# Optimization experiments

Measured on AMD Instinct MI355X. Metric: run time of the kernel, lower is better.

The kernel has to match this reference:

```python
import jax, jax.numpy as jnp
import numpy as np

B, S, D, H = 2, 2048, 1024, 16
HD = D // H
SCALE = float(np.sqrt(HD))


def setup_inputs() -> dict:
    key = jax.random.key(0)
    ks = jax.random.split(key, 11)
    std = 1.0 / np.sqrt(D)
    inp = {
        "query": jax.random.normal(ks[0], (B, S, D), dtype=jnp.float32),
        "key": jax.random.normal(ks[1], (B, S, D), dtype=jnp.float32),
        "value": jax.random.normal(ks[2], (B, S, D), dtype=jnp.float32),
        "w_q": jax.random.normal(ks[3], (D, D), dtype=jnp.float32) * std,
        "b_q": jax.random.normal(ks[4], (D,), dtype=jnp.float32) * std,
        "w_k": jax.random.normal(ks[5], (D, D), dtype=jnp.float32) * std,
        "b_k": jax.random.normal(ks[6], (D,), dtype=jnp.float32) * std,
        "w_v": jax.random.normal(ks[7], (D, D), dtype=jnp.float32) * std,
        "b_v": jax.random.normal(ks[8], (D,), dtype=jnp.float32) * std,
        "w_fc": jax.random.normal(ks[9], (D, D), dtype=jnp.float32) * std,
        "b_fc": jax.random.normal(ks[10], (D,), dtype=jnp.float32) * std,
    }
    return inp


def reference(query, key, value, w_q, b_q, w_k, b_k, w_v, b_v, w_fc, b_fc):
    # Linear projections (torch Linear: x @ W^T + b; here w_* stored as [in, out])
    Q = query @ w_q + b_q            # [B, S, D]
    K = key @ w_k + b_k
    V = value @ w_v + b_v
    # split heads -> [B, H, S, HD]
    Q = Q.reshape(B, S, H, HD).transpose(0, 2, 1, 3)
    K = K.reshape(B, S, H, HD).transpose(0, 2, 1, 3)
    V = V.reshape(B, S, H, HD).transpose(0, 2, 1, 3)
    energy = jnp.einsum('bhqd,bhkd->bhqk', Q, K) / SCALE  # [B, H, S, S]
    attn = jax.nn.softmax(energy, axis=-1)
    x = jnp.einsum('bhqk,bhkd->bhqd', attn, V)            # [B, H, S, HD]
    x = x.transpose(0, 2, 1, 3).reshape(B, S, D)
    return x @ w_fc + b_fc
```

## Files before the change

### kernel.cpp

```cpp
#include <hip/hip_runtime.h>
#include <stdint.h>

#define Bz 2
#define Sz 2048
#define Dz 1024
#define Hz 16
#define HDz 64
#define Mz (Bz*Sz)

typedef unsigned short u16;
typedef __attribute__((ext_vector_type(8))) __bf16 bf16x8;
typedef __attribute__((ext_vector_type(8))) unsigned short u16x8;
typedef __attribute__((ext_vector_type(4))) float f32x4;

#define C1 0.1803368801111243f

__device__ __forceinline__ u16 f2bf(float f) {
  union { float f; unsigned u; } v; v.f = f;
  unsigned r = v.u + 0x7fffu + ((v.u >> 16) & 1u);
  return (u16)(r >> 16);
}

__device__ __forceinline__ unsigned packbf(float a, float b) {
  unsigned ua = __builtin_bit_cast(unsigned, a);
  unsigned ub = __builtin_bit_cast(unsigned, b);
  return ((ua + 0x8000u) >> 16) | ((ub + 0x8000u) & 0xFFFF0000u);
}

__device__ __forceinline__ void async16(void* lds, const void* g) {
  __builtin_amdgcn_global_load_lds(
      (const __attribute__((address_space(1))) unsigned int*)g,
      (__attribute__((address_space(3))) unsigned int*)lds, 16, 0, 0);
}

__global__ void __launch_bounds__(256)
prep_kernel(const float* __restrict__ q, const float* __restrict__ k, const float* __restrict__ v,
            const float* __restrict__ w0, const float* __restrict__ w1,
            const float* __restrict__ w2, const float* __restrict__ w3,
            u16* __restrict__ xq, u16* __restrict__ xk, u16* __restrict__ xv,
            u16* __restrict__ Wt) {
  __shared__ __align__(16) float t[32][33];
  const int bid = blockIdx.x, tid = threadIdx.x;
  if (bid < 12288) {
    const int sel = bid >> 12;
    const int i = ((bid & 4095) << 8) + tid;
    const float* in = sel == 0 ? q : sel == 1 ? k : v;
    u16* out = sel == 0 ? xq : sel == 1 ? xk : xv;
    float4 tv = ((const float4*)in)[i];
    ((ushort4*)out)[i] = make_ushort4(f2bf(tv.x), f2bf(tv.y), f2bf(tv.z), f2bf(tv.w));
  } else {
    const int idx = bid - 12288;
    const int z = idx >> 10, r = idx & 1023;
    const int n0 = (r & 31) * 32, k0 = (r >> 5) * 32;
    const float* W = z == 0 ? w0 : z == 1 ? w1 : z == 2 ? w2 : w3;
    u16* o = Wt + (size_t)z * Dz * Dz;
    const int x = tid & 31, y = tid >> 5;
#pragma unroll
    for (int i = 0; i < 4; ++i)
      t[y + i*8][x] = W[(size_t)(k0 + y + i*8) * Dz + n0 + x];
    __syncthreads();
#pragma unroll
    for (int i = 0; i < 4; ++i)
      o[(size_t)(n0 + y + i*8) * Dz + k0 + x] = f2bf(t[x][y + i*8]);
  }
}

__global__ void __launch_bounds__(256)
gemm_qkv(const u16* __restrict__ xq, const u16* __restrict__ xk, const u16* __restrict__ xv,
         const u16* __restrict__ Wt3,
         const float* __restrict__ bq, const float* __restrict__ bk, const float* __restrict__ bv,
         u16* __restrict__ Qp, u16* __restrict__ Kp, u16* __restrict__ Vt)
{
  __shared__ __align__(16) u16 lA[128][32];
  __shared__ __align__(16) u16 lB[128][32];
  const int sel = blockIdx.x >> 3;
  const int n0 = (blockIdx.x & 7) * 128;
  const int m0 = blockIdx.y * 128;
  const u16* A = sel == 0 ? xq : sel == 1 ? xk : xv;
  const u16* Bt = Wt3 + (size_t)sel * Dz * Dz;
  const float* bias = sel == 0 ? bq : sel == 1 ? bk : bv;

  const int tid = threadIdx.x;
  const int w = tid >> 6, lane = tid & 63;
  const int wm = (w >> 1) * 64, wn = (w & 1) * 64;
  const int l16 = lane & 15, qd = lane >> 4;

  f32x4 acc[4][4];
#pragma unroll
  for (int i = 0; i < 4; ++i)
#pragma unroll
    for (int j = 0; j < 4; ++j) acc[i][j] = (f32x4){0.f, 0.f, 0.f, 0.f};

  const int r0 = tid >> 2, c0 = (tid & 3) * 8;
  const int r1 = r0 + 64;

  for (int k0 = 0; k0 < Dz; k0 += 32) {
    __syncthreads();
    async16(&lA[r0][c0], A  + (size_t)(m0 + r0) * Dz + k0 + c0);
    async16(&lB[r0][c0], Bt + (size_t)(n0 + r0) * Dz + k0 + c0);
    async16(&lA[r1][c0], A  + (size_t)(m0 + r1) * Dz + k0 + c0);
    async16(&lB[r1][c0], Bt + (size_t)(n0 + r1) * Dz + k0 + c0);
    __syncthreads();
    bf16x8 af[4], bfv[4];
#pragma unroll
    for (int t = 0; t < 4; ++t) {
      af[t]  = *(const bf16x8*)&lA[wm + t * 16 + l16][qd * 8];
      bfv[t] = *(const bf16x8*)&lB[wn + t * 16 + l16][qd * 8];
    }
#pragma unroll
    for (int mt = 0; mt < 4; ++mt)
#pragma unroll
      for (int nt = 0; nt < 4; ++nt)
        acc[mt][nt] = __builtin_amdgcn_mfma_f32_16x16x32_bf16(af[mt], bfv[nt], acc[mt][nt], 0, 0, 0);
  }

  if (sel == 2) {
    const int bq2 = m0 >> 11;
    const int s0m = (m0 & 2047) + wm;
#pragma unroll
    for (int nt = 0; nt < 4; ++nt) {
      const int n = n0 + wn + nt * 16 + l16;
      const float bvl = bias[n];
      const int h = n >> 6, hd = n & 63;
      u16* vp = Vt + (size_t)((bq2 * 16 + h) * 64 + hd) * Sz;
#pragma unroll
      for (int mt = 0; mt < 4; ++mt) {
        const int s = s0m + mt * 16 + qd * 4;
        ushort4 o = make_ushort4(f2bf(acc[mt][nt][0] + bvl), f2bf(acc[mt][nt][1] + bvl),
                                 f2bf(acc[mt][nt][2] + bvl), f2bf(acc[mt][nt][3] + bvl));
        *(ushort4*)(vp + s) = o;
      }
    }
  } else {
    u16* Cv = sel == 0 ? Qp : Kp;
#pragma unroll
    for (int nt = 0; nt < 4; ++nt) {
      const int n = n0 + wn + nt * 16 + l16;
      const float bvl = bias[n];
#pragma unroll
      for (int mt = 0; mt < 4; ++mt)
#pragma unroll
        for (int r = 0; r < 4; ++r) {
          const int m = m0 + wm + mt * 16 + qd * 4 + r;
          Cv[(size_t)m * Dz + n] = f2bf(acc[mt][nt][r] + bvl);
        }
    }
  }
}

__global__ void __launch_bounds__(256)
gemm_fc(const u16* __restrict__ A, const u16* __restrict__ Bt,
        const float* __restrict__ bias, float* __restrict__ C)
{
  __shared__ __align__(16) u16 lA[128][32];
  __shared__ __align__(16) u16 lB[64][32];
  const int m0 = blockIdx.y * 128, n0 = blockIdx.x * 64;
  const int tid = threadIdx.x;
  const int w = tid >> 6, lane = tid & 63;
  const int wm = (w >> 1) * 64, wn = (w & 1) * 32;
  const int l16 = lane & 15, qd = lane >> 4;

  f32x4 acc[4][2];
#pragma unroll
  for (int i = 0; i < 4; ++i)
#pragma unroll
    for (int j = 0; j < 2; ++j) acc[i][j] = (f32x4){0.f, 0.f, 0.f, 0.f};

  const int r0 = tid >> 2, c0 = (tid & 3) * 8;

  for (int k0 = 0; k0 < Dz; k0 += 32) {
    __syncthreads();
    async16(&lA[r0][c0],      A  + (size_t)(m0 + r0) * Dz + k0 + c0);
    async16(&lA[r0 + 64][c0], A  + (size_t)(m0 + r0 + 64) * Dz + k0 + c0);
    async16(&lB[r0][c0],      Bt + (size_t)(n0 + r0) * Dz + k0 + c0);
    __syncthreads();
    bf16x8 af[4], bfv[2];
#pragma unroll
    for (int t = 0; t < 4; ++t)
      af[t] = *(const bf16x8*)&lA[wm + t * 16 + l16][qd * 8];
#pragma unroll
    for (int t = 0; t < 2; ++t)
      bfv[t] = *(const bf16x8*)&lB[wn + t * 16 + l16][qd * 8];
#pragma unroll
    for (int mt = 0; mt < 4; ++mt)
#pragma unroll
      for (int nt = 0; nt < 2; ++nt)
        acc[mt][nt] = __builtin_amdgcn_mfma_f32_16x16x32_bf16(af[mt], bfv[nt], acc[mt][nt], 0, 0, 0);
  }

#pragma unroll
  for (int nt = 0; nt < 2; ++nt) {
    const int n = n0 + wn + nt * 16 + l16;
    const float bvl = bias[n];
#pragma unroll
    for (int mt = 0; mt < 4; ++mt)
#pragma unroll
      for (int r = 0; r < 4; ++r) {
        const int m = m0 + wm + mt * 16 + qd * 4 + r;
        C[(size_t)m * Dz + n] = acc[mt][nt][r] + bvl;
      }
  }
}

__global__ void __launch_bounds__(256, 2)
attn_kernel(const u16* __restrict__ Qp, const u16* __restrict__ Kp,
            const u16* __restrict__ Vt, u16* __restrict__ Ao)
{
  __shared__ __align__(16) u16 lK[128][72];
  __shared__ __align__(16) u16 lV[64][136];
  __shared__ __align__(16) u16 lP[4][32][136];

  const int q0 = blockIdx.x * 128;
  const int bh = blockIdx.y;
  const int b = bh >> 4, h = bh & 15;
  const int tid = threadIdx.x, w = tid >> 6, lane = tid & 63;
  const int l16 = lane & 15, qd = lane >> 4;

  const int krow = tid >> 3, kcol = (tid & 7) * 8;
  const int vrow = tid >> 4, vcol = (tid & 15) * 8;

  u16x8 kreg[4], vreg[4];
#pragma unroll
  for (int p = 0; p < 4; ++p) {
    kreg[p] = *(const u16x8*)(Kp + (size_t)(b * Sz + p * 32 + krow) * Dz + h * 64 + kcol);
    vreg[p] = *(const u16x8*)(Vt + (size_t)(bh * 64 + p * 16 + vrow) * Sz + vcol);
  }

  bf16x8 qf[2][2];
#pragma unroll
  for (int qt = 0; qt < 2; ++qt)
#pragma unroll
    for (int ksd = 0; ksd < 2; ++ksd)
      qf[qt][ksd] = *(const bf16x8*)(Qp + (size_t)(b * Sz + q0 + w * 32 + qt * 16 + l16) * Dz
                                     + h * 64 + ksd * 32 + qd * 8);

  u16x8 ob;
#pragma unroll
  for (int i = 0; i < 8; ++i) ob[i] = 0x3F80u;
  const bf16x8 onesf = __builtin_bit_cast(bf16x8, ob);

  f32x4 oacc[2][4], lacc[2];
#pragma unroll
  for (int i = 0; i < 2; ++i) {
    lacc[i] = (f32x4){0.f, 0.f, 0.f, 0.f};
#pragma unroll
    for (int j = 0; j < 4; ++j) oacc[i][j] = (f32x4){0.f, 0.f, 0.f, 0.f};
  }

  for (int t = 0; t < Sz / 128; ++t) {
    __syncthreads();
#pragma unroll
    for (int p = 0; p < 4; ++p) {
      *(u16x8*)&lK[p * 32 + krow][kcol] = kreg[p];
      *(u16x8*)&lV[p * 16 + vrow][vcol] = vreg[p];
    }
    if (t + 1 < Sz / 128) {
      const int kv = (t + 1) * 128;
#pragma unroll
      for (int p = 0; p < 4; ++p) {
        kreg[p] = *(const u16x8*)(Kp + (size_t)(b * Sz + kv + p * 32 + krow) * Dz + h * 64 + kcol);
        vreg[p] = *(const u16x8*)(Vt + (size_t)(bh * 64 + p * 16 + vrow) * Sz + kv + vcol);
      }
    }
    __syncthreads();

    f32x4 st[8][2];
#pragma unroll
    for (int i = 0; i < 8; ++i)
#pragma unroll
      for (int j = 0; j < 2; ++j) st[i][j] = (f32x4){0.f, 0.f, 0.f, 0.f};
#pragma unroll
    for (int ksd = 0; ksd < 2; ++ksd) {
      bf16x8 kf[8];
#pragma unroll
      for (int kvt = 0; kvt < 8; ++kvt)
        kf[kvt] = *(const bf16x8*)&lK[kvt * 16 + l16][ksd * 32 + qd * 8];
#pragma unroll
      for (int kvt = 0; kvt < 8; ++kvt)
#pragma unroll
        for (int qt = 0; qt < 2; ++qt)
          st[kvt][qt] = __builtin_amdgcn_mfma_f32_16x16x32_bf16(kf[kvt], qf[qt][ksd], st[kvt][qt], 0, 0, 0);
    }

#pragma unroll
    for (int kvt = 0; kvt < 8; ++kvt)
#pragma unroll
      for (int qt = 0; qt < 2; ++qt) {
        float e0 = exp2f(st[kvt][qt][0] * C1);
        float e1 = exp2f(st[kvt][qt][1] * C1);
        float e2 = exp2f(st[kvt][qt][2] * C1);
        float e3 = exp2f(st[kvt][qt][3] * C1);
        uint2 pk;
        pk.x = packbf(e0, e1);
        pk.y = packbf(e2, e3);
        *(uint2*)&lP[w][qt * 16 + l16][kvt * 16 + qd * 4] = pk;
      }

#pragma unroll
    for (int ks = 0; ks < 4; ++ks) {
      bf16x8 pa[2], vb[4];
      pa[0] = *(const bf16x8*)&lP[w][l16     ][ks * 32 + qd * 8];
      pa[1] = *(const bf16x8*)&lP[w][16 + l16][ks * 32 + qd * 8];
#pragma unroll
      for (int nt = 0; nt < 4; ++nt)
        vb[nt] = *(const bf16x8*)&lV[nt * 16 + l16][ks * 32 + qd * 8];
#pragma unroll
      for (int mt = 0; mt < 2; ++mt) {
#pragma unroll
        for (int nt = 0; nt < 4; ++nt)
          oacc[mt][nt] = __builtin_amdgcn_mfma_f32_16x16x32_bf16(pa[mt], vb[nt], oacc[mt][nt], 0, 0, 0);
        lacc[mt] = __builtin_amdgcn_mfma_f32_16x16x32_bf16(pa[mt], onesf, lacc[mt], 0, 0, 0);
      }
    }
  }

#pragma unroll
  for (int mt = 0; mt < 2; ++mt)
#pragma unroll
    for (int r = 0; r < 4; ++r) {
      const float inv = 1.0f / lacc[mt][r];
      const int row = q0 + w * 32 + mt * 16 + qd * 4 + r;
#pragma unroll
      for (int nt = 0; nt < 4; ++nt) {
        const int col = h * 64 + nt * 16 + l16;
        Ao[(size_t)(b * Sz + row) * Dz + col] = f2bf(oacc[mt][nt][r] * inv);
      }
    }
}

extern "C" void kernel_launch(void* const* d_in, const int* in_sizes, int n_in,
                              void* d_out, int out_size, void* d_ws, size_t ws_size,
                              hipStream_t stream) {
  const float* query = (const float*)d_in[0];
  const float* key   = (const float*)d_in[1];
  const float* value = (const float*)d_in[2];
  const float* w_q  = (const float*)d_in[3];
  const float* b_q  = (const float*)d_in[4];
  const float* w_k  = (const float*)d_in[5];
  const float* b_k  = (const float*)d_in[6];
  const float* w_v  = (const float*)d_in[7];
  const float* b_v  = (const float*)d_in[8];
  const float* w_fc = (const float*)d_in[9];
  const float* b_fc = (const float*)d_in[10];
  float* out = (float*)d_out;

  const size_t XE = (size_t)Mz * Dz;
  const size_t WE = (size_t)Dz * Dz;
  u16* Xq  = (u16*)d_ws;
  u16* Xk  = Xq + XE;
  u16* Xv  = Xk + XE;
  u16* Wt  = Xv + XE;
  u16* Wtf = Wt + 3 * WE;
  u16* Qp  = Wt + 4 * WE;
  u16* Kp  = Qp + XE;
  u16* Vt  = Kp + XE;
  u16* Ao  = Xq;

  prep_kernel<<<16384, 256, 0, stream>>>(query, key, value, w_q, w_k, w_v, w_fc,
                                         Xq, Xk, Xv, Wt);

  gemm_qkv<<<dim3(24, Mz / 128), 256, 0, stream>>>(Xq, Xk, Xv, Wt, b_q, b_k, b_v, Qp, Kp, Vt);

  attn_kernel<<<dim3(Sz / 128, Bz * Hz), 256, 0, stream>>>(Qp, Kp, Vt, Ao);

  gemm_fc<<<dim3(Dz / 64, Mz / 128), 256, 0, stream>>>(Ao, Wtf, b_fc, out);
}
```

Before: 259.5 us.

## Keep P in registers via shuffles, compute transposed PV, split V transpose out

The attention kernel no longer stages the exponentiated scores P through a per-wave LDS buffer. Instead it packs P in registers and uses cross-lane shuffles to build the MFMA B operand, computing O^T = V^T P^T so the score layout matches without a transpose. Dropping the LDS P buffer allows raising launch bounds to 3 blocks per SM. The QKV GEMM now writes V in plain row layout, and a new small kernel transposes it, which adds one launch and an extra pass over V. The shuffles add ALU/permute work in the inner loop.

```diff
diff --git a/kernel.cpp b/kernel.cpp
--- a/kernel.cpp
+++ b/kernel.cpp
@@ -25,6 +25,12 @@
   unsigned ua = __builtin_bit_cast(unsigned, a);
   unsigned ub = __builtin_bit_cast(unsigned, b);
   return ((ua + 0x8000u) >> 16) | ((ub + 0x8000u) & 0xFFFF0000u);
+}
+
+__device__ __forceinline__ bf16x8 mk8(unsigned a, unsigned b, unsigned c, unsigned d) {
+  union { unsigned u[4]; bf16x8 v; } x;
+  x.u[0] = a; x.u[1] = b; x.u[2] = c; x.u[3] = d;
+  return x.v;
 }
 
 __device__ __forceinline__ void async16(void* lds, const void* g) {
@@ -66,10 +72,34 @@
 }
 
 __global__ void __launch_bounds__(256)
+vtrans_kernel(const u16* __restrict__ Vp, u16* __restrict__ Vt) {
+  __shared__ __align__(16) u16 t[64][72];
+  int s0 = blockIdx.x * 64, bh = blockIdx.y;
+  int b = bh >> 4;
+  int h = bh & 15;
+  int tid = threadIdx.x;
+#pragma unroll
+  for (int p = 0; p < 4; ++p) {
+    int c = p * 256 + tid;
+    int row = c >> 4, off = (c & 15) * 4;
+    ushort4 v = *(const ushort4*)(Vp + (size_t)(b * Sz + s0 + row) * Dz + h * 64 + off);
+    *(ushort4*)&t[row][off] = v;
+  }
+  __syncthreads();
+#pragma unroll
+  for (int p = 0; p < 4; ++p) {
+    int c = p * 256 + tid;
+    int d = c >> 4, sc = (c & 15) * 4;
+    ushort4 v = make_ushort4(t[sc + 0][d], t[sc + 1][d], t[sc + 2][d], t[sc + 3][d]);
+    *(ushort4*)(Vt + (size_t)(bh * 64 + d) * Sz + s0 + sc) = v;
+  }
+}
+
+__global__ void __launch_bounds__(256)
 gemm_qkv(const u16* __restrict__ xq, const u16* __restrict__ xk, const u16* __restrict__ xv,
          const u16* __restrict__ Wt3,
          const float* __restrict__ bq, const float* __restrict__ bk, const float* __restrict__ bv,
-         u16* __restrict__ Qp, u16* __restrict__ Kp, u16* __restrict__ Vt)
+         u16* __restrict__ Qp, u16* __restrict__ Kp, u16* __restrict__ Vp)
 {
   __shared__ __align__(16) u16 lA[128][32];
   __shared__ __align__(16) u16 lB[128][32];
@@ -79,6 +109,7 @@
   const u16* A = sel == 0 ? xq : sel == 1 ? xk : xv;
   const u16* Bt = Wt3 + (size_t)sel * Dz * Dz;
   const float* bias = sel == 0 ? bq : sel == 1 ? bk : bv;
+  u16* Cv = sel == 0 ? Qp : sel == 1 ? Kp : Vp;
 
   const int tid = threadIdx.x;
   const int w = tid >> 6, lane = tid & 63;
@@ -114,37 +145,17 @@
         acc[mt][nt] = __builtin_amdgcn_mfma_f32_16x16x32_bf16(af[mt], bfv[nt], acc[mt][nt], 0, 0, 0);
   }
 
-  if (sel == 2) {
-    const int bq2 = m0 >> 11;
-    const int s0m = (m0 & 2047) + wm;
-#pragma unroll
-    for (int nt = 0; nt < 4; ++nt) {
-      const int n = n0 + wn + nt * 16 + l16;
-      const float bvl = bias[n];
-      const int h = n >> 6, hd = n & 63;
-      u16* vp = Vt + (size_t)((bq2 * 16 + h) * 64 + hd) * Sz;
-#pragma unroll
-      for (int mt = 0; mt < 4; ++mt) {
-        const int s = s0m + mt * 16 + qd * 4;
-        ushort4 o = make_ushort4(f2bf(acc[mt][nt][0] + bvl), f2bf(acc[mt][nt][1] + bvl),
-                                 f2bf(acc[mt][nt][2] + bvl), f2bf(acc[mt][nt][3] + bvl));
-        *(ushort4*)(vp + s) = o;
+#pragma unroll
+  for (int nt = 0; nt < 4; ++nt) {
+    const int n = n0 + wn + nt * 16 + l16;
+    const float bvl = bias[n];
+#pragma unroll
+    for (int mt = 0; mt < 4; ++mt)
+#pragma unroll
+      for (int r = 0; r < 4; ++r) {
+        const int m = m0 + wm + mt * 16 + qd * 4 + r;
+        Cv[(size_t)m * Dz + n] = f2bf(acc[mt][nt][r] + bvl);
       }
-    }
-  } else {
-    u16* Cv = sel == 0 ? Qp : Kp;
-#pragma unroll
-    for (int nt = 0; nt < 4; ++nt) {
-      const int n = n0 + wn + nt * 16 + l16;
-      const float bvl = bias[n];
-#pragma unroll
-      for (int mt = 0; mt < 4; ++mt)
-#pragma unroll
-        for (int r = 0; r < 4; ++r) {
-          const int m = m0 + wm + mt * 16 + qd * 4 + r;
-          Cv[(size_t)m * Dz + n] = f2bf(acc[mt][nt][r] + bvl);
-        }
-    }
   }
 }
 
@@ -202,13 +213,12 @@
   }
 }
 
-__global__ void __launch_bounds__(256, 2)
+__global__ void __launch_bounds__(256, 3)
 attn_kernel(const u16* __restrict__ Qp, const u16* __restrict__ Kp,
             const u16* __restrict__ Vt, u16* __restrict__ Ao)
 {
   __shared__ __align__(16) u16 lK[128][72];
   __shared__ __align__(16) u16 lV[64][136];
-  __shared__ __align__(16) u16 lP[4][32][136];
 
   const int q0 = blockIdx.x * 128;
   const int bh = blockIdx.y;
@@ -237,15 +247,18 @@
   u16x8 ob;
 #pragma unroll
   for (int i = 0; i < 8; ++i) ob[i] = 0x3F80u;
-  const bf16x8 onesf = __builtin_bit_cast(bf16x8, ob);
-
-  f32x4 oacc[2][4], lacc[2];
-#pragma unroll
-  for (int i = 0; i < 2; ++i) {
-    lacc[i] = (f32x4){0.f, 0.f, 0.f, 0.f};
-#pragma unroll
-    for (int j = 0; j < 4; ++j) oacc[i][j] = (f32x4){0.f, 0.f, 0.f, 0.f};
-  }
+  const bf16x8 onesA = __builtin_bit_cast(bf16x8, ob);
+
+  const int sidx0 = ((qd & 1) * 2) * 16 + l16;
+
+  f32x4 oaccT[4][2];
+  f32x4 laccT[2];
+#pragma unroll
+  for (int mt = 0; mt < 4; ++mt)
+#pragma unroll
+    for (int qt = 0; qt < 2; ++qt) oaccT[mt][qt] = (f32x4){0.f, 0.f, 0.f, 0.f};
+  laccT[0] = (f32x4){0.f, 0.f, 0.f, 0.f};
+  laccT[1] = (f32x4){0.f, 0.f, 0.f, 0.f};
 
   for (int t = 0; t < Sz / 128; ++t) {
     __syncthreads();
@@ -283,48 +296,58 @@
     }
 
 #pragma unroll
-    for (int kvt = 0; kvt < 8; ++kvt)
+    for (int ks = 0; ks < 4; ++ks) {
+      unsigned pkl[2][2][2];
+#pragma unroll
+      for (int j = 0; j < 2; ++j)
+#pragma unroll
+        for (int qt = 0; qt < 2; ++qt) {
+          const f32x4 s4 = st[2 * ks + j][qt];
+          float e0 = exp2f(s4[0] * C1);
+          float e1 = exp2f(s4[1] * C1);
+          float e2 = exp2f(s4[2] * C1);
+          float e3 = exp2f(s4[3] * C1);
+          pkl[j][qt][0] = packbf(e0, e1);
+          pkl[j][qt][1] = packbf(e2, e3);
+        }
+
+      bf16x8 vfA[4];
+#pragma unroll
+      for (int mt = 0; mt < 4; ++mt)
+        vfA[mt] = *(const bf16x8*)&lV[mt * 16 + l16][ks * 32 + qd * 8];
+
 #pragma unroll
       for (int qt = 0; qt < 2; ++qt) {
-        float e0 = exp2f(st[kvt][qt][0] * C1);
-        float e1 = exp2f(st[kvt][qt][1] * C1);
-        float e2 = exp2f(st[kvt][qt][2] * C1);
-        float e3 = exp2f(st[kvt][qt][3] * C1);
-        uint2 pk;
-        pk.x = packbf(e0, e1);
-        pk.y = packbf(e2, e3);
-        *(uint2*)&lP[w][qt * 16 + l16][kvt * 16 + qd * 4] = pk;
+        unsigned v[4];
+#pragma unroll
+        for (int i = 0; i < 4; ++i) {
+          const int si = sidx0 + (i >> 1) * 16;
+          unsigned tA = (unsigned)__shfl((int)pkl[0][qt][i & 1], si);
+          unsigned tB = (unsigned)__shfl((int)pkl[1][qt][i & 1], si);
+          v[i] = (qd & 2) ? tB : tA;
+        }
+        const bf16x8 pb = mk8(v[0], v[1], v[2], v[3]);
+#pragma unroll
+        for (int mt = 0; mt < 4; ++mt)
+          oaccT[mt][qt] = __builtin_amdgcn_mfma_f32_16x16x32_bf16(vfA[mt], pb, oaccT[mt][qt], 0, 0, 0);
+        laccT[qt] = __builtin_amdgcn_mfma_f32_16x16x32_bf16(onesA, pb, laccT[qt], 0, 0, 0);
       }
-
-#pragma unroll
-    for (int ks = 0; ks < 4; ++ks) {
-      bf16x8 pa[2], vb[4];
-      pa[0] = *(const bf16x8*)&lP[w][l16     ][ks * 32 + qd * 8];
-      pa[1] = *(const bf16x8*)&lP[w][16 + l16][ks * 32 + qd * 8];
-#pragma unroll
-      for (int nt = 0; nt < 4; ++nt)
-        vb[nt] = *(const bf16x8*)&lV[nt * 16 + l16][ks * 32 + qd * 8];
-#pragma unroll
-      for (int mt = 0; mt < 2; ++mt) {
-#pragma unroll
-        for (int nt = 0; nt < 4; ++nt)
-          oacc[mt][nt] = __builtin_amdgcn_mfma_f32_16x16x32_bf16(pa[mt], vb[nt], oacc[mt][nt], 0, 0, 0);
-        lacc[mt] = __builtin_amdgcn_mfma_f32_16x16x32_bf16(pa[mt], onesf, lacc[mt], 0, 0, 0);
-      }
-    }
-  }
-
-#pragma unroll
-  for (int mt = 0; mt < 2; ++mt)
-#pragma unroll
-    for (int r = 0; r < 4; ++r) {
-      const float inv = 1.0f / lacc[mt][r];
-      const int row = q0 + w * 32 + mt * 16 + qd * 4 + r;
-#pragma unroll
-      for (int nt = 0; nt < 4; ++nt) {
-        const int col = h * 64 + nt * 16 + l16;
-        Ao[(size_t)(b * Sz + row) * Dz + col] = f2bf(oacc[mt][nt][r] * inv);
-      }
+    }
+  }
+
+  float inv[2];
+  inv[0] = 1.0f / laccT[0][0];
+  inv[1] = 1.0f / laccT[1][0];
+#pragma unroll
+  for (int mt = 0; mt < 4; ++mt)
+#pragma unroll
+    for (int qt = 0; qt < 2; ++qt) {
+      const int q = b * Sz + q0 + w * 32 + qt * 16 + l16;
+      ushort4 o = make_ushort4(f2bf(oaccT[mt][qt][0] * inv[qt]),
+                               f2bf(oaccT[mt][qt][1] * inv[qt]),
+                               f2bf(oaccT[mt][qt][2] * inv[qt]),
+                               f2bf(oaccT[mt][qt][3] * inv[qt]));
+      *(ushort4*)(Ao + (size_t)q * Dz + h * 64 + mt * 16 + qd * 4) = o;
     }
 }
 
@@ -353,13 +376,16 @@
   u16* Wtf = Wt + 3 * WE;
   u16* Qp  = Wt + 4 * WE;
   u16* Kp  = Qp + XE;
-  u16* Vt  = Kp + XE;
+  u16* Vp  = Kp + XE;
+  u16* Vt  = Xk;
   u16* Ao  = Xq;
 
   prep_kernel<<<16384, 256, 0, stream>>>(query, key, value, w_q, w_k, w_v, w_fc,
                                          Xq, Xk, Xv, Wt);
 
-  gemm_qkv<<<dim3(24, Mz / 128), 256, 0, stream>>>(Xq, Xk, Xv, Wt, b_q, b_k, b_v, Qp, Kp, Vt);
+  gemm_qkv<<<dim3(24, Mz / 128), 256, 0, stream>>>(Xq, Xk, Xv, Wt, b_q, b_k, b_v, Qp, Kp, Vp);
+
+  vtrans_kernel<<<dim3(Sz / 64, Bz * Hz), 256, 0, stream>>>(Vp, Vt);
 
   attn_kernel<<<dim3(Sz / 128, Bz * Hz), 256, 0, stream>>>(Qp, Kp, Vt, Ao);
 
```

Result: slower. 299.6 us (+15.5%).
